# Optimization experiments

Measured on AMD Instinct MI355X. Metric: run time of the kernel, lower is better.

Reference implementation:

```python
import jax, jax.numpy as jnp
import numpy as np
import math

L_LAYERS = 4
EMBED = 512
HEADS = 8
FFN = 2048
EPS = 1e-20
PAD_IDX = 0


def sinusoidal_table(num_embeddings, embedding_dim, padding_idx=0):
    half = embedding_dim // 2
    freq = jnp.exp(jnp.arange(half, dtype=jnp.float32) * (-math.log(10000.0) / (half - 1)))
    ang = jnp.arange(num_embeddings, dtype=jnp.float32)[:, None] * freq[None, :]
    emb = jnp.concatenate([jnp.sin(ang), jnp.cos(ang)], axis=1)
    if padding_idx is not None:
        emb = emb.at[padding_idx].set(0.0)
    return emb  # [num_embeddings, embedding_dim]


def layer_norm(x, g, b):
    mu = jnp.mean(x, axis=-1, keepdims=True)
    var = jnp.mean((x - mu) ** 2, axis=-1, keepdims=True)
    return (x - mu) * jax.lax.rsqrt(var + EPS) * g + b


def mha(x_q, x_kv, Wqkv, bqkv, Wo, bo, mask):
    """Custom attention: scaled scores, multiplicative mask, GLOBAL min-max norm (no softmax)."""
    T, B, C = x_q.shape
    S = x_kv.shape[0]
    hd = C // HEADS
    scale = hd ** -0.5
    q = x_q @ Wqkv[:C].T + bqkv[:C]
    k = x_kv @ Wqkv[C:2 * C].T + bqkv[C:2 * C]
    v = x_kv @ Wqkv[2 * C:].T + bqkv[2 * C:]
    q = q * scale
    # [T,B,C] -> [B*H, T, hd]
    q = q.reshape(T, B * HEADS, hd).transpose(1, 0, 2)
    k = k.reshape(S, B * HEADS, hd).transpose(1, 0, 2)
    v = v.reshape(S, B * HEADS, hd).transpose(1, 0, 2)
    w = jnp.einsum('bth,bsh->bts', q, k)  # [B*H, T, S]
    if mask is not None:
        w = w * mask[None, :, :]
    # global min-max normalization (as in the torch source)
    w = (w - jnp.min(w)) / (jnp.max(w) - jnp.min(w))
    a = jnp.einsum('bts,bsh->bth', w, v)  # [B*H, T, hd]
    a = a.transpose(1, 0, 2).reshape(T, B, C)
    return a @ Wo.T + bo


def setup_inputs() -> dict:
    key = jax.random.key(0)
    ks = iter(jax.random.split(key, 32))
    T, B, C, F, L = 2048, 2, EMBED, FFN, L_LAYERS
    d = {}
    d['x'] = jax.random.normal(next(ks), (T, B, C), dtype=jnp.float32)
    d['enc_out'] = jax.random.normal(next(ks), (T, B, C), dtype=jnp.float32)
    d['tokens'] = jax.random.randint(next(ks), (B, T), 0, 32000, dtype=jnp.int64 if jax.config.read('jax_enable_x64') else jnp.int32)
    sd = C ** -0.5
    d['self_Wqkv'] = jax.random.normal(next(ks), (L, 3 * C, C)) * sd
    d['self_bqkv'] = jnp.zeros((L, 3 * C))
    d['self_Wo'] = jax.random.normal(next(ks), (L, C, C)) * sd
    d['self_bo'] = jnp.zeros((L, C))
    d['cross_Wqkv'] = jax.random.normal(next(ks), (L, 3 * C, C)) * sd
    d['cross_bqkv'] = jnp.zeros((L, 3 * C))
    d['cross_Wo'] = jax.random.normal(next(ks), (L, C, C)) * sd
    d['cross_bo'] = jnp.zeros((L, C))
    d['fc1_w'] = jax.random.normal(next(ks), (L, F, C)) * sd
    d['fc1_b'] = jnp.zeros((L, F))
    d['fc2_w'] = jax.random.normal(next(ks), (L, C, F)) * (F ** -0.5)
    d['fc2_b'] = jnp.zeros((L, C))
    d['ln1_g'] = jnp.ones((L, C)); d['ln1_b'] = jnp.zeros((L, C))
    d['ln2_g'] = jnp.ones((L, C)); d['ln2_b'] = jnp.zeros((L, C))
    d['ln3_g'] = jnp.ones((L, C)); d['ln3_b'] = jnp.zeros((L, C))
    return d


def _forward(x, enc_out, tokens, self_Wqkv, self_bqkv, self_Wo, self_bo,
             cross_Wqkv, cross_bqkv, cross_Wo, cross_bo,
             fc1_w, fc1_b, fc2_w, fc2_b, ln1_g, ln1_b, ln2_g, ln2_b, ln3_g, ln3_b):
    T, B, C = x.shape
    # sinusoidal positional embedding (make_positions with padding_idx=0, no left pad)
    table = sinusoidal_table(PAD_IDX + 1 + T, C, PAD_IDX)
    pos = jnp.where(tokens != PAD_IDX, jnp.arange(1, T + 1)[None, :], 0)  # [B, T]
    pe = table[pos]  # [B, T, C]
    x = x + pe.transpose(1, 0, 2)
    # multiplicative future mask: tril of ones
    fmask = jnp.tril(jnp.ones((T, T), dtype=x.dtype))
    for l in range(L_LAYERS):
        # self-attention
        res = x
        x = mha(x, x, self_Wqkv[l], self_bqkv[l], self_Wo[l], self_bo[l], fmask)
        x = layer_norm(res + x, ln1_g[l], ln1_b[l])
        # cross-attention (no mask)
        res = x
        x = mha(x, enc_out, cross_Wqkv[l], cross_bqkv[l], cross_Wo[l], cross_bo[l], None)
        x = layer_norm(res + x, ln2_g[l], ln2_b[l])
        # FFN
        res = x
        h = jax.nn.relu(x @ fc1_w[l].T + fc1_b[l])
        x = h @ fc2_w[l].T + fc2_b[l]
        x = layer_norm(res + x, ln3_g[l], ln3_b[l])
    return x


def reference(x, enc_out, tokens, self_Wqkv, self_bqkv, self_Wo, self_bo,
              cross_Wqkv, cross_bqkv, cross_Wo, cross_bo,
              fc1_w, fc1_b, fc2_w, fc2_b, ln1_g, ln1_b, ln2_g, ln2_b, ln3_g, ln3_b):
    return _forward(x, enc_out, tokens, self_Wqkv, self_bqkv, self_Wo, self_bo,
                    cross_Wqkv, cross_bqkv, cross_Wo, cross_bo,
                    fc1_w, fc1_b, fc2_w, fc2_b, ln1_g, ln1_b, ln2_g, ln2_b, ln3_g, ln3_b)
```

## Files before the change

kernel.cpp:

```cpp
#include <hip/hip_runtime.h>
#include <math.h>

typedef __bf16 bf16;
typedef unsigned short u16;
typedef unsigned int u32;
typedef __bf16 bf16x8 __attribute__((ext_vector_type(8)));
typedef float f32x4 __attribute__((ext_vector_type(4)));

#define T_SEQ 2048
#define NB    2
#define CE    512
#define HD    64
#define ROWS  4096
#define LDT   40
#define LDA   72

#define MFMA16(a,b,c) __builtin_amdgcn_mfma_f32_16x16x32_bf16((a),(b),(c),0,0,0)

static __device__ __forceinline__ int xcd_swz(int id, int n) {
  int q = n >> 3, r = n & 7;
  int x = id & 7, o = id >> 3;
  return (x < r) ? (x * (q + 1) + o) : (r * (q + 1) + (x - r) * q + o);
}

static __device__ __forceinline__ float ldf(const void* src, size_t eoff, bool f32) {
  return f32 ? ((const float*)src)[eoff] : (float)((const bf16*)src)[eoff];
}

static __device__ __forceinline__ u32 fenc(float f) {
  u32 u = __float_as_uint(f);
  return (u & 0x80000000u) ? ~u : (u | 0x80000000u);
}
static __device__ __forceinline__ float fdec(u32 u) {
  u32 v = (u & 0x80000000u) ? (u & 0x7fffffffu) : ~u;
  return __uint_as_float(v);
}

__global__ __launch_bounds__(256) void sniff(const u16* __restrict__ xs,
                                             const int* __restrict__ toks,
                                             int* __restrict__ flags)
{
  const int tid = threadIdx.x;
  int crazy = 0, ze = 0;
  for (int i = tid; i < 4096; i += 256) {
    int e = (xs[i] >> 7) & 0xFF;
    if (e >= 141) crazy++;
    if (((i & 1) == 0) && (xs[i] == 0)) ze++;
  }
  int zc = 0;
  for (int i = tid; i < 1024; i += 256)
    if (toks[2 * i + 1] == 0) zc++;
  __shared__ int r1[4], r2[4], r3[4];
#pragma unroll
  for (int o = 32; o; o >>= 1) {
    crazy += __shfl_down(crazy, o); ze += __shfl_down(ze, o); zc += __shfl_down(zc, o);
  }
  if ((tid & 63) == 0) { r1[tid >> 6] = crazy; r2[tid >> 6] = ze; r3[tid >> 6] = zc; }
  __syncthreads();
  if (tid == 0) {
    int c = r1[0] + r1[1] + r1[2] + r1[3];
    int z = r2[0] + r2[1] + r2[2] + r2[3];
    int t = r3[0] + r3[1] + r3[2] + r3[3];
    flags[0] = (z > 1500 || c > 64) ? 1 : 0;
    flags[1] = (t > 900) ? 1 : 0;
    flags[3] = 0;
    flags[4] = 0;
  }
}

__global__ __launch_bounds__(256) void probe_lo(const void* w0, const void* w1, const void* w2,
                                                const void* w3, const void* w4, const void* w5,
                                                const void* w6,
                                                int* __restrict__ flags)
{
  if (flags[0] == 0) return;
  const int m = blockIdx.y;
  const void* srcs[7] = {w0, w1, w2, w3, w4, w5, w6};
  const int sizes[7]  = {3145728, 1048576, 3145728, 1048576, 4194304, 4194304, 2097152};
  const float4* p = (const float4*)srcs[m];
  const int n4 = sizes[m] >> 2;
  bool nz = false;
  for (int i = blockIdx.x * 256 + threadIdx.x; i < n4; i += 128 * 256) {
    float4 v = p[i];
    nz = nz || (v.x != (float)(bf16)v.x) || (v.y != (float)(bf16)v.y)
            || (v.z != (float)(bf16)v.z) || (v.w != (float)(bf16)v.w);
  }
  unsigned long long mv = __ballot(nz);
  if ((threadIdx.x & 63) == 0 && mv)
    atomicOr(&flags[(m == 6) ? 3 : 4], 1);
}

__global__ __launch_bounds__(256) void posembed(const void* __restrict__ xsrc,
                                                const int* __restrict__ toks,
                                                const int* __restrict__ flags,
                                                float* __restrict__ xf,
                                                bf16* __restrict__ xh, bf16* __restrict__ xl)
{
  const bool f32 = flags[0] != 0;
  const bool tok64 = flags[1] != 0;
  const int row = blockIdx.x;
  const int t = row >> 1, b = row & 1;
  const int tix = b * T_SEQ + t;
  const int tok = tok64 ? toks[2 * tix] : toks[tix];
  const int p = (tok != 0) ? (t + 1) : 0;
  const float kf = -0.0361193740f;
  for (int c = threadIdx.x; c < CE; c += 256) {
    float pe = 0.0f;
    if (p != 0) {
      int i = (c < 256) ? c : (c - 256);
      float freq = expf((float)i * kf);
      float ang = (float)p * freq;
      pe = (c < 256) ? sinf(ang) : cosf(ang);
    }
    float v = ldf(xsrc, (size_t)row * CE + c, f32) + pe;
    size_t o = (size_t)row * CE + c;
    xf[o] = v;
    bf16 hi = (bf16)v;
    xh[o] = hi; xl[o] = (bf16)(v - (float)hi);
  }
}

template<int OUTM, bool BIAS>
__global__ __launch_bounds__(256) void gemm_bb(const bf16* __restrict__ A1h, const bf16* __restrict__ A1l,
                                               const void* __restrict__ A2,
                                               const void* __restrict__ Braw, long long bOff,
                                               const void* __restrict__ bias, size_t biasOff,
                                               const int* __restrict__ flags,
                                               float* __restrict__ Cf,
                                               bf16* __restrict__ Coh, bf16* __restrict__ Col,
                                               int N, int K, int kspan, int nbx, int nbxA,
                                               long long partStride)
{
  __shared__ __align__(16) bf16 Ah[128 * LDT];
  __shared__ __align__(16) bf16 Al[128 * LDT];
  __shared__ __align__(16) bf16 Bh[64 * LDT];
  __shared__ __align__(16) bf16 Bl[64 * LDT];
  const int id = xcd_swz((int)blockIdx.x, (int)gridDim.x);
  const int per_z = nbx * 32;
  const int zz = id / per_z;
  const int rem = id - zz * per_z;
  const int by = rem / nbx, bx = rem - by * nbx;
  const bool bfl = flags[0] != 0;
  const bool blo = bfl && (flags[4] != 0);
  const bool aSplit = (bx < nbxA);
  const bool a2lo = bfl && (flags[3] != 0);
  const bool alo = aSplit ? true : a2lo;
  const int tid = threadIdx.x;
  const int m0 = by * 128, n0 = bx * 64;
  const int srA = tid >> 1, skA = (tid & 1) * 16;
  const int srB = tid >> 2, skB = (tid & 3) * 8;
  const int wid = tid >> 6, lane = tid & 63;
  const int wm = (wid >> 1) * 64, wn = (wid & 1) * 32;
  const int fr = lane & 15, fk = (lane >> 4) * 8;
  const int kb = zz * kspan;
  const int ke = (kb + kspan < K) ? (kb + kspan) : K;
  f32x4 acc[4][2] = {};

  uint4 ra0, ra1, ra2, ra3, rb0, rb1;
  auto loadA = [&](int k0) {
    size_t g = (size_t)(m0 + srA) * K + k0 + skA;
    if (aSplit) {
      const uint4* p = (const uint4*)(A1h + g); ra0 = p[0]; ra1 = p[1];
      const uint4* q = (const uint4*)(A1l + g); ra2 = q[0]; ra3 = q[1];
    } else if (bfl) {
      const uint4* p = (const uint4*)((const float*)A2 + g);
      ra0 = p[0]; ra1 = p[1]; ra2 = p[2]; ra3 = p[3];
    } else {
      const uint4* p = (const uint4*)((const bf16*)A2 + g); ra0 = p[0]; ra1 = p[1];
    }
  };
  auto loadB = [&](int k0) {
    size_t g = (size_t)bOff + (size_t)(n0 + srB) * K + k0 + skB;
    if (bfl) {
      const uint4* p = (const uint4*)((const float*)Braw + g); rb0 = p[0]; rb1 = p[1];
    } else {
      rb0 = *(const uint4*)((const bf16*)Braw + g);
    }
  };
  auto storeA = [&]() {
    if (aSplit) {
      *(uint4*)&Ah[srA * LDT + skA]     = ra0;
      *(uint4*)&Ah[srA * LDT + skA + 8] = ra1;
      *(uint4*)&Al[srA * LDT + skA]     = ra2;
      *(uint4*)&Al[srA * LDT + skA + 8] = ra3;
    } else if (bfl) {
      float v[16];
      const float* f0 = (const float*)&ra0; const float* f1 = (const float*)&ra1;
      const float* f2 = (const float*)&ra2; const float* f3 = (const float*)&ra3;
#pragma unroll
      for (int q = 0; q < 4; q++) { v[q] = f0[q]; v[4+q] = f1[q]; v[8+q] = f2[q]; v[12+q] = f3[q]; }
      bf16x8 h0, h1;
#pragma unroll
      for (int q = 0; q < 8; q++) { h0[q] = (bf16)v[q]; h1[q] = (bf16)v[8+q]; }
      *(bf16x8*)&Ah[srA * LDT + skA]     = h0;
      *(bf16x8*)&Ah[srA * LDT + skA + 8] = h1;
      if (a2lo) {
        bf16x8 l0, l1;
#pragma unroll
        for (int q = 0; q < 8; q++) {
          l0[q] = (bf16)(v[q]   - (float)h0[q]);
          l1[q] = (bf16)(v[8+q] - (float)h1[q]);
        }
        *(bf16x8*)&Al[srA * LDT + skA]     = l0;
        *(bf16x8*)&Al[srA * LDT + skA + 8] = l1;
      }
    } else {
      *(uint4*)&Ah[srA * LDT + skA]     = ra0;
      *(uint4*)&Ah[srA * LDT + skA + 8] = ra1;
    }
  };
  auto storeB = [&]() {
    if (bfl) {
      float v[8];
      const float* f0 = (const float*)&rb0; const float* f1 = (const float*)&rb1;
#pragma unroll
      for (int q = 0; q < 4; q++) { v[q] = f0[q]; v[4+q] = f1[q]; }
      bf16x8 h0;
#pragma unroll
      for (int q = 0; q < 8; q++) h0[q] = (bf16)v[q];
      *(bf16x8*)&Bh[srB * LDT + skB] = h0;
      if (blo) {
        bf16x8 l0;
#pragma unroll
        for (int q = 0; q < 8; q++) l0[q] = (bf16)(v[q] - (float)h0[q]);
        *(bf16x8*)&Bl[srB * LDT + skB] = l0;
      }
    } else {
      *(uint4*)&Bh[srB * LDT + skB] = rb0;
    }
  };

  loadA(kb); loadB(kb);
  for (int k0 = kb; k0 < ke; k0 += 32) {
    __syncthreads();
    storeA(); storeB();
    __syncthreads();
    if (k0 + 32 < ke) { loadA(k0 + 32); loadB(k0 + 32); }
    bf16x8 ah[4], bh2[2];
#pragma unroll
    for (int i = 0; i < 4; i++) ah[i] = *(const bf16x8*)&Ah[(wm + i*16 + fr) * LDT + fk];
#pragma unroll
    for (int j = 0; j < 2; j++) bh2[j] = *(const bf16x8*)&Bh[(wn + j*16 + fr) * LDT + fk];
#pragma unroll
    for (int i = 0; i < 4; i++)
#pragma unroll
      for (int j = 0; j < 2; j++)
        acc[i][j] = MFMA16(ah[i], bh2[j], acc[i][j]);
    if (alo) {
      bf16x8 al[4];
#pragma unroll
      for (int i = 0; i < 4; i++) al[i] = *(const bf16x8*)&Al[(wm + i*16 + fr) * LDT + fk];
#pragma unroll
      for (int i = 0; i < 4; i++)
#pragma unroll
        for (int j = 0; j < 2; j++)
          acc[i][j] = MFMA16(al[i], bh2[j], acc[i][j]);
    }
    if (blo) {
      bf16x8 bl[2];
#pragma unroll
      for (int j = 0; j < 2; j++) bl[j] = *(const bf16x8*)&Bl[(wn + j*16 + fr) * LDT + fk];
#pragma unroll
      for (int i = 0; i < 4; i++)
#pragma unroll
        for (int j = 0; j < 2; j++)
          acc[i][j] = MFMA16(ah[i], bl[j], acc[i][j]);
    }
  }
  const int orow0 = m0 + wm + (lane >> 4) * 4;
  const int ocol0 = n0 + wn + (lane & 15);
  if (OUTM == 0) {
    float* Cp = Cf + (long long)zz * partStride;
    const bool addb = BIAS && (zz == 0);
#pragma unroll
    for (int j = 0; j < 2; j++) {
      int col = ocol0 + j * 16;
      float bv = addb ? ldf(bias, biasOff + col, flags[0] != 0) : 0.0f;
#pragma unroll
      for (int i = 0; i < 4; i++)
#pragma unroll
        for (int r = 0; r < 4; r++)
          Cp[(size_t)(orow0 + i * 16 + r) * N + col] = acc[i][j][r] + bv;
    }
  } else {
#pragma unroll
    for (int j = 0; j < 2; j++) {
      int col = ocol0 + j * 16;
      float bv = ldf(bias, biasOff + col, flags[0] != 0);
#pragma unroll
      for (int i = 0; i < 4; i++)
#pragma unroll
        for (int r = 0; r < 4; r++) {
          float vv = fmaxf(acc[i][j][r] + bv, 0.0f);
          bf16 hi = (bf16)vv;
          size_t o = (size_t)(orow0 + i * 16 + r) * N + col;
          Coh[o] = hi; Col[o] = (bf16)(vv - (float)hi);
        }
    }
  }
}

__global__ __launch_bounds__(256) void prep_kv(const float* __restrict__ base, int ld,
                                               int kofs0, int vofs0,
                                               bf16* __restrict__ kh, bf16* __restrict__ kl,
                                               bf16* __restrict__ vth, bf16* __restrict__ vtl,
                                               float* __restrict__ vcs,
                                               u32* __restrict__ mmf_u)
{
  __shared__ float ts[64 * 65];
  const int bh = blockIdx.x, s0 = blockIdx.y * 64;
  const int b = bh >> 3, hq = bh & 7;
  const int kofs = kofs0 + hq * HD, vofs = vofs0 + hq * HD;
  const int tid = threadIdx.x;
  if (tid == 0) { mmf_u[0] = 0xFFFFFFFFu; mmf_u[1] = 0u; }
#pragma unroll
  for (int it = 0; it < 16; ++it) {
    int idx = it * 256 + tid, r = idx >> 6, d = idx & 63;
    size_t rowb = (size_t)((s0 + r) * NB + b) * ld;
    float v = base[rowb + kofs + d];
    bf16 hi = (bf16)v;
    size_t o = ((size_t)bh * T_SEQ + s0 + r) * 64 + d;
    kh[o] = hi; kl[o] = (bf16)(v - (float)hi);
    ts[r * 65 + d] = base[rowb + vofs + d];
  }
  __syncthreads();
  const int d = tid >> 2, sseg = (tid & 3) * 16;
  bf16x8 hv0, lv0, hv1, lv1;
#pragma unroll
  for (int q = 0; q < 8; ++q) {
    float v0 = ts[(sseg + q) * 65 + d];
    float v1 = ts[(sseg + 8 + q) * 65 + d];
    bf16 h0 = (bf16)v0, h1 = (bf16)v1;
    hv0[q] = h0; lv0[q] = (bf16)(v0 - (float)h0);
    hv1[q] = h1; lv1[q] = (bf16)(v1 - (float)h1);
  }
  size_t o = ((size_t)bh * 64 + d) * T_SEQ + s0 + sseg;
  *(bf16x8*)&vth[o]     = hv0;
  *(bf16x8*)&vth[o + 8] = hv1;
  *(bf16x8*)&vtl[o]     = lv0;
  *(bf16x8*)&vtl[o + 8] = lv1;
  if (tid < 64) {
    float s = 0.0f;
    for (int j = 0; j < 64; ++j) s += ts[j * 65 + tid];
    vcs[((size_t)bh * 32 + blockIdx.y) * 64 + tid] = s;
  }
}

__device__ __forceinline__ int remap_ty(int ty) { return (ty < 16) ? ty : 47 - ty; }

template<bool MASK>
__global__ __launch_bounds__(256) void fattn(const float* __restrict__ qbase, int qld, int qofs0,
                                             const bf16* __restrict__ kh, const bf16* __restrict__ kl,
                                             const bf16* __restrict__ vth, const bf16* __restrict__ vtl,
                                             u32* __restrict__ mmf_u,
                                             bf16* __restrict__ pvh, bf16* __restrict__ pvl)
{
  __shared__ __align__(16) bf16 Kh[64 * LDA], Kl[64 * LDA];
  __shared__ __align__(16) bf16 Vh[64 * LDA], Vl[64 * LDA];
  __shared__ __align__(16) bf16 Ph[64 * LDA], Pl[64 * LDA];
  __shared__ float rn[4], rx[4];
  const int id = xcd_swz((int)blockIdx.x, 512);
  const int bh = id >> 5;
  const int tyr = remap_ty(id & 31);
  const int t0 = tyr * 64;
  const int b = bh >> 3, hq = bh & 7;
  const int qofs = qofs0 + hq * HD;
  const int tid = threadIdx.x;
  const int wv = tid >> 6, lane = tid & 63;
  const int g = lane >> 4, c = lane & 15;
  bf16x8 qh[2], ql[2];
  {
    size_t qrow = (size_t)((t0 + wv * 16 + c) * NB + b) * qld + qofs;
#pragma unroll
    for (int ks = 0; ks < 2; ++ks) {
      float4 f0 = *(const float4*)&qbase[qrow + ks * 32 + g * 8];
      float4 f1 = *(const float4*)&qbase[qrow + ks * 32 + g * 8 + 4];
      float v[8] = {f0.x, f0.y, f0.z, f0.w, f1.x, f1.y, f1.z, f1.w};
#pragma unroll
      for (int q = 0; q < 8; ++q) {
        float s = v[q] * 0.125f;
        bf16 hi = (bf16)s;
        qh[ks][q] = hi; ql[ks][q] = (bf16)(s - (float)hi);
      }
    }
  }
  const int cr = tid >> 2, cs = (tid & 3) * 16;
  uint4 rkh0, rkh1, rkl0, rkl1, rvh0, rvh1, rvl0, rvl1;
  auto loadKV = [&](int s0) {
    size_t go = ((size_t)bh * T_SEQ + s0 + cr) * 64 + cs;
    rkh0 = *(const uint4*)&kh[go]; rkh1 = *(const uint4*)&kh[go + 8];
    rkl0 = *(const uint4*)&kl[go]; rkl1 = *(const uint4*)&kl[go + 8];
    size_t gv = ((size_t)bh * 64 + cr) * T_SEQ + s0 + cs;
    rvh0 = *(const uint4*)&vth[gv]; rvh1 = *(const uint4*)&vth[gv + 8];
    rvl0 = *(const uint4*)&vtl[gv]; rvl1 = *(const uint4*)&vtl[gv + 8];
  };
  auto storeKV = [&]() {
    const int base = cr * LDA + cs;
    *(uint4*)&Kh[base]     = rkh0; *(uint4*)&Kh[base + 8] = rkh1;
    *(uint4*)&Kl[base]     = rkl0; *(uint4*)&Kl[base + 8] = rkl1;
    *(uint4*)&Vh[base]     = rvh0; *(uint4*)&Vh[base + 8] = rvh1;
    *(uint4*)&Vl[base]     = rvl0; *(uint4*)&Vl[base + 8] = rvl1;
  };
  float mn = 1e30f, mx = -1e30f;
  f32x4 o4[4] = {};
  const int nch = MASK ? (tyr + 1) : 32;
  loadKV(0);
  for (int sc = 0; sc < nch; ++sc) {
    const int s0 = sc * 64;
    __syncthreads();
    storeKV();
    __syncthreads();
    if (sc + 1 < nch) loadKV(s0 + 64);
    f32x4 a4[4] = {};
#pragma unroll
    for (int ks = 0; ks < 2; ++ks) {
#pragma unroll
      for (int j = 0; j < 4; ++j) {
        bf16x8 kfh = *(const bf16x8*)&Kh[(j * 16 + c) * LDA + ks * 32 + g * 8];
        bf16x8 kfl = *(const bf16x8*)&Kl[(j * 16 + c) * LDA + ks * 32 + g * 8];
        a4[j] = MFMA16(qh[ks], kfh, a4[j]);
        a4[j] = MFMA16(ql[ks], kfh, a4[j]);
        a4[j] = MFMA16(qh[ks], kfl, a4[j]);
      }
    }
#pragma unroll
    for (int j = 0; j < 4; ++j)
#pragma unroll
      for (int r = 0; r < 4; ++r) {
        int tl = wv * 16 + g * 4 + r;
        int sl = j * 16 + c;
        float w = a4[j][r];
        if (MASK && (s0 + sl) > (t0 + tl)) w = 0.0f;
        mn = fminf(mn, w); mx = fmaxf(mx, w);
        bf16 wh = (bf16)w;
        Ph[tl * LDA + sl] = wh;
        Pl[tl * LDA + sl] = (bf16)(w - (float)wh);
      }
    asm volatile("s_waitcnt lgkmcnt(0)" ::: "memory");
    __builtin_amdgcn_sched_barrier(0);
#pragma unroll
    for (int ks = 0; ks < 2; ++ks) {
      bf16x8 pah = *(const bf16x8*)&Ph[(wv * 16 + c) * LDA + ks * 32 + g * 8];
      bf16x8 pal = *(const bf16x8*)&Pl[(wv * 16 + c) * LDA + ks * 32 + g * 8];
#pragma unroll
      for (int j = 0; j < 4; ++j) {
        bf16x8 vfh = *(const bf16x8*)&Vh[(j * 16 + c) * LDA + ks * 32 + g * 8];
        bf16x8 vfl = *(const bf16x8*)&Vl[(j * 16 + c) * LDA + ks * 32 + g * 8];
        o4[j] = MFMA16(pah, vfh, o4[j]);
        o4[j] = MFMA16(pal, vfh, o4[j]);
        o4[j] = MFMA16(pah, vfl, o4[j]);
      }
    }
  }
#pragma unroll
  for (int j = 0; j < 4; ++j)
#pragma unroll
    for (int r = 0; r < 4; ++r) {
      int tl = wv * 16 + g * 4 + r;
      int dl = j * 16 + c;
      float val = o4[j][r];
      bf16 hi = (bf16)val;
      size_t o = (size_t)((t0 + tl) * NB + b) * CE + hq * HD + dl;
      pvh[o] = hi; pvl[o] = (bf16)(val - (float)hi);
    }
#pragma unroll
  for (int o = 32; o; o >>= 1) { mn = fminf(mn, __shfl_down(mn, o)); mx = fmaxf(mx, __shfl_down(mx, o)); }
  if (lane == 0) { rn[wv] = mn; rx[wv] = mx; }
  __syncthreads();
  if (tid == 0) {
    float bmn = fminf(fminf(rn[0], rn[1]), fminf(rn[2], rn[3]));
    float bmx = fmaxf(fmaxf(rx[0], rx[1]), fmaxf(rx[2], rx[3]));
    atomicMin(&mmf_u[0], fenc(bmn));
    atomicMax(&mmf_u[1], fenc(bmx));
  }
}

__global__ __launch_bounds__(256) void wo_term(const u32* __restrict__ mmf_u,
                                               const float* __restrict__ vcs,
                                               const void* __restrict__ Wo, size_t woOff,
                                               const void* __restrict__ bo, size_t boOff,
                                               const int* __restrict__ flags,
                                               float* __restrict__ term)
{
  __shared__ float vs[512];
  const bool fl = flags[0] != 0;
  const int tid = threadIdx.x;
  const float mn = fdec(mmf_u[0]);
  const float inv = 1.0f / (fdec(mmf_u[1]) - mn);
  const float cmn = mn * inv;
  const int b = blockIdx.x >> 5;
  for (int k = tid; k < 512; k += 256) {
    int h = k >> 6, d = k & 63;
    float s = 0.0f;
#pragma unroll
    for (int ch = 0; ch < 32; ++ch)
      s += vcs[(size_t)((b * 8 + h) * 32 + ch) * 64 + d];
    vs[k] = s;
  }
  __syncthreads();
  const int out = blockIdx.x * 16 + (tid >> 4);
  const int c = out & 511;
  const int k0 = (tid & 15) * 32;
  float s = 0.0f;
#pragma unroll 8
  for (int k = 0; k < 32; ++k)
    s += vs[k0 + k] * ldf(Wo, woOff + (size_t)c * 512 + k0 + k, fl);
  s += __shfl_down(s, 8); s += __shfl_down(s, 4); s += __shfl_down(s, 2); s += __shfl_down(s, 1);
  if ((tid & 15) == 0)
    term[out] = -cmn * s + ldf(bo, boOff + c, fl);
}

template<int NP, bool AFF, bool SPLIT>
__global__ __launch_bounds__(256) void ln_sum(const float* __restrict__ res,
                                              const float* __restrict__ p, long long pstride,
                                              const void* __restrict__ g, const void* __restrict__ be,
                                              size_t goff, const int* __restrict__ flags,
                                              const u32* __restrict__ mmf_u,
                                              const float* __restrict__ term,
                                              float* __restrict__ xfo,
                                              bf16* __restrict__ xh, bf16* __restrict__ xl)
{
  __shared__ float red[4];
  const bool fl = flags[0] != 0;
  const int tid = threadIdx.x;
  const size_t base = (size_t)blockIdx.x * CE;
  float pa = 0.0f, pb = 0.0f;
#pragma unroll
  for (int k = 0; k < NP; k++) {
    pa += p[(long long)k * pstride + base + tid];
    pb += p[(long long)k * pstride + base + tid + 256];
  }
  float a, b2;
  if (AFF) {
    const float mnv = fdec(mmf_u[0]);
    const float inv = 1.0f / (fdec(mmf_u[1]) - mnv);
    const int b = blockIdx.x & 1;
    a  = res[base + tid]       + inv * pa + term[b * 512 + tid];
    b2 = res[base + tid + 256] + inv * pb + term[b * 512 + tid + 256];
  } else {
    a  = res[base + tid]       + pa;
    b2 = res[base + tid + 256] + pb;
  }
  float s = a + b2;
#pragma unroll
  for (int o = 32; o; o >>= 1) s += __shfl_down(s, o);
  if ((tid & 63) == 0) red[tid >> 6] = s;
  __syncthreads();
  float mu = (red[0] + red[1] + red[2] + red[3]) * (1.0f / 512.0f);
  __syncthreads();
  float da = a - mu, db = b2 - mu;
  float q = da * da + db * db;
#pragma unroll
  for (int o = 32; o; o >>= 1) q += __shfl_down(q, o);
  if ((tid & 63) == 0) red[tid >> 6] = q;
  __syncthreads();
  float var = (red[0] + red[1] + red[2] + red[3]) * (1.0f / 512.0f);
  float rs = rsqrtf(var + 1e-20f);
  float o1 = da * rs * ldf(g, goff + tid, fl)       + ldf(be, goff + tid, fl);
  float o2 = db * rs * ldf(g, goff + tid + 256, fl) + ldf(be, goff + tid + 256, fl);
  xfo[base + tid]       = o1;
  xfo[base + tid + 256] = o2;
  if (SPLIT) {
    bf16 h1 = (bf16)o1, h2 = (bf16)o2;
    xh[base + tid]       = h1; xl[base + tid]       = (bf16)(o1 - (float)h1);
    xh[base + tid + 256] = h2; xl[base + tid + 256] = (bf16)(o2 - (float)h2);
  }
}

extern "C" void kernel_launch(void* const* d_in, const int* in_sizes, int n_in,
                              void* d_out, int out_size, void* d_ws, size_t ws_size,
                              hipStream_t stream)
{
  (void)in_sizes; (void)n_in; (void)out_size; (void)ws_size;
  const void* x_in   = d_in[0];
  const void* enc_in = d_in[1];
  const int*  tokens = (const int*)d_in[2];
  const void* sWqkv = d_in[3];
  const void* sbqkv = d_in[4];
  const void* sWo   = d_in[5];
  const void* sbo   = d_in[6];
  const void* cWqkv = d_in[7];
  const void* cbqkv = d_in[8];
  const void* cWo   = d_in[9];
  const void* cbo   = d_in[10];
  const void* fc1w  = d_in[11];
  const void* fc1b  = d_in[12];
  const void* fc2w  = d_in[13];
  const void* fc2b  = d_in[14];
  const void* ln1g  = d_in[15];
  const void* ln1b  = d_in[16];
  const void* ln2g  = d_in[17];
  const void* ln2b  = d_in[18];
  const void* ln3g  = d_in[19];
  const void* ln3b  = d_in[20];

  char* ws = (char*)d_ws;
  size_t off = 0;
  auto alloc = [&](size_t bytes) -> char* {
    char* p = ws + off;
    off += (bytes + 255) & ~(size_t)255;
    return p;
  };
  int*   flags   = (int*)  alloc(256);
  u32*   mmf_u   = (u32*)  alloc(256);
  float* term    = (float*)alloc(1024 * 4);
  float* xf      = (float*)alloc((size_t)ROWS * CE * 4);
  bf16*  xh      = (bf16*) alloc((size_t)ROWS * CE * 2);
  bf16*  xl      = (bf16*) alloc((size_t)ROWS * CE * 2);
  float* qkv     = (float*)alloc((size_t)ROWS * 2048 * 4);
  bf16*  pvh     = (bf16*) alloc((size_t)ROWS * CE * 2);
  bf16*  pvl     = (bf16*) alloc((size_t)ROWS * CE * 2);
  float* pblk    = (float*)alloc((size_t)ROWS * CE * 4 * 4);
  bf16*  khb     = (bf16*) alloc((size_t)16 * T_SEQ * 64 * 2);
  bf16*  klb     = (bf16*) alloc((size_t)16 * T_SEQ * 64 * 2);
  bf16*  vth     = (bf16*) alloc((size_t)16 * 64 * T_SEQ * 2);
  bf16*  vtl     = (bf16*) alloc((size_t)16 * 64 * T_SEQ * 2);
  float* vcs     = (float*)alloc((size_t)16 * 32 * 64 * 4);
  bf16* hh = (bf16*)qkv;
  bf16* hl = (bf16*)qkv + (size_t)ROWS * 2048;
  const long long PS_FULL = (long long)ROWS * CE;

  sniff<<<1, 256, 0, stream>>>((const u16*)x_in, tokens, flags);
  probe_lo<<<dim3(128, 7), 256, 0, stream>>>(sWqkv, sWo, cWqkv, cWo, fc1w, fc2w, enc_in, flags);
  posembed<<<ROWS, 256, 0, stream>>>(x_in, tokens, flags, xf, xh, xl);

  for (int l = 0; l < 4; l++) {
    gemm_bb<0, true><<<768, 256, 0, stream>>>(
        xh, xl, xh,
        sWqkv, (long long)l * 786432,
        sbqkv, (size_t)l * 1536, flags,
        qkv, nullptr, nullptr, 1536, 512, 512, 24, 24, 0);
    prep_kv<<<dim3(16, 32), 256, 0, stream>>>(qkv, 1536, 512, 1024, khb, klb, vth, vtl, vcs, mmf_u);
    fattn<true><<<512, 256, 0, stream>>>(qkv, 1536, 0, khb, klb, vth, vtl, mmf_u, pvh, pvl);
    wo_term<<<64, 256, 0, stream>>>(mmf_u, vcs, sWo, (size_t)l * 262144, sbo, (size_t)l * 512,
                                    flags, term);
    gemm_bb<0, false><<<1024, 256, 0, stream>>>(
        pvh, pvl, pvh,
        sWo, (long long)l * 262144,
        sbo, 0, flags,
        pblk, nullptr, nullptr, 512, 512, 128, 8, 8, PS_FULL);
    ln_sum<4, true, true><<<ROWS, 256, 0, stream>>>(
        xf, pblk, PS_FULL, ln1g, ln1b, (size_t)l * 512, flags, mmf_u, term, xf, xh, xl);

    gemm_bb<0, true><<<768, 256, 0, stream>>>(
        xh, xl, enc_in,
        cWqkv, (long long)l * 786432,
        cbqkv, (size_t)l * 1536, flags,
        qkv, nullptr, nullptr, 1536, 512, 512, 24, 8, 0);
    prep_kv<<<dim3(16, 32), 256, 0, stream>>>(qkv, 1536, 512, 1024, khb, klb, vth, vtl, vcs, mmf_u);
    fattn<false><<<512, 256, 0, stream>>>(qkv, 1536, 0, khb, klb, vth, vtl, mmf_u, pvh, pvl);
    wo_term<<<64, 256, 0, stream>>>(mmf_u, vcs, cWo, (size_t)l * 262144, cbo, (size_t)l * 512,
                                    flags, term);
    gemm_bb<0, false><<<1024, 256, 0, stream>>>(
        pvh, pvl, pvh,
        cWo, (long long)l * 262144,
        cbo, 0, flags,
        pblk, nullptr, nullptr, 512, 512, 128, 8, 8, PS_FULL);
    ln_sum<4, true, true><<<ROWS, 256, 0, stream>>>(
        xf, pblk, PS_FULL, ln2g, ln2b, (size_t)l * 512, flags, mmf_u, term, xf, xh, xl);

    gemm_bb<1, true><<<1024, 256, 0, stream>>>(
        xh, xl, xh,
        fc1w, (long long)l * 1048576,
        fc1b, (size_t)l * 2048, flags,
        nullptr, hh, hl, 2048, 512, 512, 32, 32, 0);
    gemm_bb<0, true><<<1024, 256, 0, stream>>>(
        hh, hl, hh,
        fc2w, (long long)l * 1048576,
        fc2b, (size_t)l * 512, flags,
        pblk, nullptr, nullptr, 512, 2048, 512, 8, 8, PS_FULL);
    if (l == 3) {
      ln_sum<4, false, false><<<ROWS, 256, 0, stream>>>(
          xf, pblk, PS_FULL, ln3g, ln3b, (size_t)l * 512, flags, nullptr, nullptr,
          (float*)d_out, nullptr, nullptr);
    } else {
      ln_sum<4, false, true><<<ROWS, 256, 0, stream>>>(
          xf, pblk, PS_FULL, ln3g, ln3b, (size_t)l * 512, flags, nullptr, nullptr,
          xf, xh, xl);
    }
  }
}
```

Baseline: 2.288 ms.

## Load K/V MFMA fragments directly from global memory instead of staging in LDS

Result: slower. 3.571 ms (+56.1%).

```diff
diff --git a/kernel.cpp b/kernel.cpp
--- a/kernel.cpp
+++ b/kernel.cpp
@@ -355,8 +355,6 @@
                                              u32* __restrict__ mmf_u,
                                              bf16* __restrict__ pvh, bf16* __restrict__ pvl)
 {
-  __shared__ __align__(16) bf16 Kh[64 * LDA], Kl[64 * LDA];
-  __shared__ __align__(16) bf16 Vh[64 * LDA], Vl[64 * LDA];
   __shared__ __align__(16) bf16 Ph[64 * LDA], Pl[64 * LDA];
   __shared__ float rn[4], rx[4];
   const int id = xcd_swz((int)blockIdx.x, 512);
@@ -384,43 +382,28 @@
       }
     }
   }
-  const int cr = tid >> 2, cs = (tid & 3) * 16;
-  uint4 rkh0, rkh1, rkl0, rkl1, rvh0, rvh1, rvl0, rvl1;
-  auto loadKV = [&](int s0) {
-    size_t go = ((size_t)bh * T_SEQ + s0 + cr) * 64 + cs;
-    rkh0 = *(const uint4*)&kh[go]; rkh1 = *(const uint4*)&kh[go + 8];
-    rkl0 = *(const uint4*)&kl[go]; rkl1 = *(const uint4*)&kl[go + 8];
-    size_t gv = ((size_t)bh * 64 + cr) * T_SEQ + s0 + cs;
-    rvh0 = *(const uint4*)&vth[gv]; rvh1 = *(const uint4*)&vth[gv + 8];
-    rvl0 = *(const uint4*)&vtl[gv]; rvl1 = *(const uint4*)&vtl[gv + 8];
-  };
-  auto storeKV = [&]() {
-    const int base = cr * LDA + cs;
-    *(uint4*)&Kh[base]     = rkh0; *(uint4*)&Kh[base + 8] = rkh1;
-    *(uint4*)&Kl[base]     = rkl0; *(uint4*)&Kl[base + 8] = rkl1;
-    *(uint4*)&Vh[base]     = rvh0; *(uint4*)&Vh[base + 8] = rvh1;
-    *(uint4*)&Vl[base]     = rvl0; *(uint4*)&Vl[base + 8] = rvl1;
-  };
+  const size_t kbase = (size_t)bh * T_SEQ * 64;
+  const size_t vbase = (size_t)bh * 64 * T_SEQ;
   float mn = 1e30f, mx = -1e30f;
   f32x4 o4[4] = {};
   const int nch = MASK ? (tyr + 1) : 32;
-  loadKV(0);
   for (int sc = 0; sc < nch; ++sc) {
     const int s0 = sc * 64;
-    __syncthreads();
-    storeKV();
-    __syncthreads();
-    if (sc + 1 < nch) loadKV(s0 + 64);
     f32x4 a4[4] = {};
 #pragma unroll
     for (int ks = 0; ks < 2; ++ks) {
+      bf16x8 kfh[4], kfl[4];
 #pragma unroll
       for (int j = 0; j < 4; ++j) {
-        bf16x8 kfh = *(const bf16x8*)&Kh[(j * 16 + c) * LDA + ks * 32 + g * 8];
-        bf16x8 kfl = *(const bf16x8*)&Kl[(j * 16 + c) * LDA + ks * 32 + g * 8];
-        a4[j] = MFMA16(qh[ks], kfh, a4[j]);
-        a4[j] = MFMA16(ql[ks], kfh, a4[j]);
-        a4[j] = MFMA16(qh[ks], kfl, a4[j]);
+        size_t go = kbase + (size_t)(s0 + j * 16 + c) * 64 + ks * 32 + g * 8;
+        kfh[j] = *(const bf16x8*)&kh[go];
+        kfl[j] = *(const bf16x8*)&kl[go];
+      }
+#pragma unroll
+      for (int j = 0; j < 4; ++j) {
+        a4[j] = MFMA16(qh[ks], kfh[j], a4[j]);
+        a4[j] = MFMA16(ql[ks], kfh[j], a4[j]);
+        a4[j] = MFMA16(qh[ks], kfl[j], a4[j]);
       }
     }
 #pragma unroll
@@ -442,13 +425,18 @@
     for (int ks = 0; ks < 2; ++ks) {
       bf16x8 pah = *(const bf16x8*)&Ph[(wv * 16 + c) * LDA + ks * 32 + g * 8];
       bf16x8 pal = *(const bf16x8*)&Pl[(wv * 16 + c) * LDA + ks * 32 + g * 8];
+      bf16x8 vfh[4], vfl[4];
 #pragma unroll
       for (int j = 0; j < 4; ++j) {
-        bf16x8 vfh = *(const bf16x8*)&Vh[(j * 16 + c) * LDA + ks * 32 + g * 8];
-        bf16x8 vfl = *(const bf16x8*)&Vl[(j * 16 + c) * LDA + ks * 32 + g * 8];
-        o4[j] = MFMA16(pah, vfh, o4[j]);
-        o4[j] = MFMA16(pal, vfh, o4[j]);
-        o4[j] = MFMA16(pah, vfl, o4[j]);
+        size_t gv = vbase + (size_t)(j * 16 + c) * T_SEQ + s0 + ks * 32 + g * 8;
+        vfh[j] = *(const bf16x8*)&vth[gv];
+        vfl[j] = *(const bf16x8*)&vtl[gv];
+      }
+#pragma unroll
+      for (int j = 0; j < 4; ++j) {
+        o4[j] = MFMA16(pah, vfh[j], o4[j]);
+        o4[j] = MFMA16(pal, vfh[j], o4[j]);
+        o4[j] = MFMA16(pah, vfl[j], o4[j]);
       }
     }
   }
```
